# Kernel optimization log

Hardware: AMD Instinct MI355X
Metric: run time of the kernel (lower is better)

Reference implementation:

```python
import jax, jax.numpy as jnp
import numpy as np
from jax import lax

NT, NGRID, NX, H, NY = 365, 2000, 16, 256, 1


def setup_inputs() -> dict:
    key = jax.random.key(0)
    ks = jax.random.split(key, 7)
    s_x = 1.0 / np.sqrt(NX)
    s_h = 1.0 / np.sqrt(H)
    return {
        "x": jax.random.normal(ks[0], (NT, NGRID, NX), dtype=jnp.float32),
        # untied per-gate weights, gate order: [input, forget, cell, output]
        "wx": jax.random.uniform(ks[1], (4, NX, H), jnp.float32, -s_x, s_x),
        "wh": jax.random.uniform(ks[2], (4, H, H), jnp.float32, -s_h, s_h),
        "b": jax.random.uniform(ks[3], (4, H), jnp.float32, -s_h, s_h),
        "w_lin": jax.random.uniform(ks[4], (H, NY), jnp.float32, -s_h, s_h),
        "b_lin": jax.random.uniform(ks[5], (NY,), jnp.float32, -s_h, s_h),
    }


def reference(x, wx, wh, b, w_lin, b_lin):
    # x: [T, N, nx]. Precompute all input-to-gate projections in one big GEMM
    # (the time loop only needs the recurrent h @ wh part).
    ngrid = x.shape[1]
    hid = wh.shape[-1]
    xg = jnp.einsum('tni,gih->tngh', x, wx) + b  # [T, N, 4, H]

    def step(carry, xg_t):
        h, c = carry
        g = xg_t + jnp.einsum('nh,gho->ngo', h, wh)  # [N, 4, H]
        i = jax.nn.sigmoid(g[:, 0])
        f = jax.nn.sigmoid(g[:, 1])
        gt = jnp.tanh(g[:, 2])
        o = jax.nn.sigmoid(g[:, 3])
        c = f * c + i * gt
        h = o * jnp.tanh(c)
        return (h, c), h

    h0 = jnp.zeros((ngrid, hid), dtype=x.dtype)
    c0 = jnp.zeros((ngrid, hid), dtype=x.dtype)
    _, hs = lax.scan(step, (h0, c0), xg)  # hs: [T, N, H]
    out = hs @ w_lin + b_lin  # [T, N, ny]
    return out
```

## Files before the change

### kernel.cpp

```cpp
#include <hip/hip_runtime.h>
#include <cstddef>

#define TSTEPS 365
#define NGRID_ 2000
#define NX_ 16
#define H_ 256
#define CPB 16
#define NBLK (NGRID_ / CPB)

typedef __attribute__((ext_vector_type(8))) short short8v;
typedef __attribute__((ext_vector_type(4))) float f32x4;

__device__ __forceinline__ unsigned short f2bf(float f) {
    unsigned int u = __float_as_uint(f);
    u += 0x7fffu + ((u >> 16) & 1u);
    return (unsigned short)(u >> 16);
}
__device__ __forceinline__ float bf2f(unsigned short s) {
    return __uint_as_float(((unsigned int)s) << 16);
}
__device__ __forceinline__ float sigmoid_f(float v) {
    return 1.0f / (1.0f + __expf(-v));
}
__device__ __forceinline__ float tanh_f(float v) {
    return 1.0f - 2.0f / (__expf(2.0f * v) + 1.0f);
}

#define WH_WORDS (64 * 8 * 64)
#define WX_WORDS (64 * 64)

__global__ __launch_bounds__(256) void pack_weights(
    const float* __restrict__ wh, const float* __restrict__ wx,
    unsigned short* __restrict__ pb)
{
    int tid = blockIdx.x * 256 + threadIdx.x;
    short8v sv;
    if (tid < WH_WORDS) {
        int lane = tid & 63;
        int kt   = (tid >> 6) & 7;
        int gu   = tid >> 9;
        int g    = gu >> 4;
        int ncol = ((gu & 15) << 4) | (lane & 15);
        int kb   = kt * 32 + ((lane >> 4) << 3);
#pragma unroll
        for (int j = 0; j < 8; ++j)
            sv[j] = (short)f2bf(wh[((size_t)(g * H_ + kb + j)) * H_ + ncol]);
        *(short8v*)(pb + (size_t)tid * 8) = sv;
    } else if (tid < WH_WORDS + WX_WORDS) {
        int t2   = tid - WH_WORDS;
        int lane = t2 & 63;
        int gu   = t2 >> 6;
        int g    = gu >> 4;
        int ncol = ((gu & 15) << 4) | (lane & 15);
        int kkb  = (lane >> 4) << 3;
#pragma unroll
        for (int j = 0; j < 8; ++j) {
            int k = (kkb + j) & 15;
            sv[j] = (short)f2bf(wx[((size_t)(g * NX_ + k)) * H_ + ncol]);
        }
        *(short8v*)(pb + (size_t)tid * 8) = sv;
    }
}

__global__ __launch_bounds__(512) void lstm_mfma(
    const float* __restrict__ x,
    const float* __restrict__ b,
    const float* __restrict__ wlin,
    const float* __restrict__ blin,
    const unsigned short* __restrict__ pb,
    float* __restrict__ out)
{
    __shared__ __align__(16) unsigned short Ah[2][32][16][8];
    __shared__ __align__(16) unsigned short Al[2][32][16][8];
    __shared__ __align__(16) unsigned short Ax[2][4][16][8];
    __shared__ float red[2][8][16];

    const int tid = threadIdx.x;
    const int w   = tid >> 6;
    const int l   = tid & 63;
    const int lg  = l >> 4;
    const int ln  = l & 15;
    const int c0  = blockIdx.x * CPB;

    float bias[4][2], wl[2];
#pragma unroll
    for (int g = 0; g < 4; ++g)
#pragma unroll
        for (int ut = 0; ut < 2; ++ut)
            bias[g][ut] = b[g * H_ + w * 32 + ut * 16 + ln];
    wl[0] = wlin[w * 32 + ln];
    wl[1] = wlin[w * 32 + 16 + ln];
    const float bl = blin[0];

    const unsigned short* BX = pb + (size_t)WH_WORDS * 8;

    {
        uint4 z = make_uint4(0, 0, 0, 0);
        ((uint4*)&Ah[0][0][0][0])[tid] = z;
        ((uint4*)&Al[0][0][0][0])[tid] = z;
    }
    if (tid < 256) {
        int cell = tid >> 4, nx = tid & 15;
        float v = x[((size_t)(c0 + cell)) * NX_ + nx];
        unsigned short hi = f2bf(v);
        unsigned short lo = f2bf(v - bf2f(hi));
        Ax[0][nx >> 3][cell][nx & 7] = hi;
        Ax[0][2 + (nx >> 3)][cell][nx & 7] = lo;
    }
    __syncthreads();

    f32x4 acc[4][2];
    float c_st[2][4];
#pragma unroll
    for (int ut = 0; ut < 2; ++ut)
#pragma unroll
        for (int r = 0; r < 4; ++r) c_st[ut][r] = 0.0f;

#pragma unroll 1
    for (int t = 0; t < TSTEPS; ++t) {
        const int rb = t & 1, wb = rb ^ 1;

#pragma unroll
        for (int g = 0; g < 4; ++g)
#pragma unroll
            for (int ut = 0; ut < 2; ++ut) {
                f32x4 a0 = {bias[g][ut], bias[g][ut], bias[g][ut], bias[g][ut]};
                acc[g][ut] = a0;
            }

#pragma unroll
        for (int kt = 0; kt < 8; ++kt) {
            short8v ah = *(const short8v*)&Ah[rb][kt * 4 + lg][ln][0];
            short8v al = *(const short8v*)&Al[rb][kt * 4 + lg][ln][0];
#pragma unroll
            for (int g = 0; g < 4; ++g)
#pragma unroll
                for (int ut = 0; ut < 2; ++ut) {
                    int gu = (g << 4) | (w * 2 + ut);
                    short8v bb = *(const short8v*)(pb + ((size_t)(gu * 8 + kt) * 64 + l) * 8);
                    acc[g][ut] = __builtin_amdgcn_mfma_f32_16x16x32_bf16(ah, bb, acc[g][ut], 0, 0, 0);
                    acc[g][ut] = __builtin_amdgcn_mfma_f32_16x16x32_bf16(al, bb, acc[g][ut], 0, 0, 0);
                }
        }
        {
            short8v axv = *(const short8v*)&Ax[rb][lg][ln][0];
#pragma unroll
            for (int g = 0; g < 4; ++g)
#pragma unroll
                for (int ut = 0; ut < 2; ++ut) {
                    int gu = (g << 4) | (w * 2 + ut);
                    short8v bb = *(const short8v*)(BX + ((size_t)gu * 64 + l) * 8);
                    acc[g][ut] = __builtin_amdgcn_mfma_f32_16x16x32_bf16(axv, bb, acc[g][ut], 0, 0, 0);
                }
        }

        float hN[2][4];
#pragma unroll
        for (int ut = 0; ut < 2; ++ut)
#pragma unroll
            for (int r = 0; r < 4; ++r) {
                float ig = sigmoid_f(acc[0][ut][r]);
                float fg = sigmoid_f(acc[1][ut][r]);
                float gt = tanh_f(acc[2][ut][r]);
                float og = sigmoid_f(acc[3][ut][r]);
                float c  = fmaf(fg, c_st[ut][r], ig * gt);
                c_st[ut][r] = c;
                hN[ut][r]   = og * tanh_f(c);
            }

#pragma unroll
        for (int ut = 0; ut < 2; ++ut) {
            int u = w * 32 + ut * 16 + ln;
            int row = u >> 3, q = u & 7;
#pragma unroll
            for (int r = 0; r < 4; ++r) {
                int cell = lg * 4 + r;
                unsigned short hi = f2bf(hN[ut][r]);
                Ah[wb][row][cell][q] = hi;
                Al[wb][row][cell][q] = f2bf(hN[ut][r] - bf2f(hi));
            }
        }
        if (t + 1 < TSTEPS && tid < 256) {
            int cell = tid >> 4, nx = tid & 15;
            float v = x[(((size_t)(t + 1)) * NGRID_ + c0 + cell) * NX_ + nx];
            unsigned short hi = f2bf(v);
            unsigned short lo = f2bf(v - bf2f(hi));
            Ax[wb][nx >> 3][cell][nx & 7] = hi;
            Ax[wb][2 + (nx >> 3)][cell][nx & 7] = lo;
        }

        {
            float p[4];
#pragma unroll
            for (int r = 0; r < 4; ++r) {
                p[r] = fmaf(hN[0][r], wl[0], hN[1][r] * wl[1]);
#pragma unroll
                for (int off = 1; off < 16; off <<= 1)
                    p[r] += __shfl_xor(p[r], off);
            }
            if (ln == 0) {
#pragma unroll
                for (int r = 0; r < 4; ++r)
                    red[rb][w][lg * 4 + r] = p[r];
            }
        }

        __syncthreads();

        if (tid < CPB) {
            float s = bl;
#pragma unroll
            for (int w2 = 0; w2 < 8; ++w2) s += red[rb][w2][tid];
            out[(size_t)t * NGRID_ + c0 + tid] = s;
        }
    }
}

extern "C" void kernel_launch(void* const* d_in, const int* in_sizes, int n_in,
                              void* d_out, int out_size, void* d_ws, size_t ws_size,
                              hipStream_t stream) {
    const float* x    = (const float*)d_in[0];
    const float* wx   = (const float*)d_in[1];
    const float* wh   = (const float*)d_in[2];
    const float* b    = (const float*)d_in[3];
    const float* wlin = (const float*)d_in[4];
    const float* blin = (const float*)d_in[5];
    float* out = (float*)d_out;
    unsigned short* pb = (unsigned short*)d_ws;

    hipLaunchKernelGGL(pack_weights, dim3((WH_WORDS + WX_WORDS) / 256), dim3(256),
                       0, stream, wh, wx, pb);
    hipLaunchKernelGGL(lstm_mfma, dim3(NBLK), dim3(512), 0, stream,
                       x, b, wlin, blin, pb, out);
}
```

Measured before the change: 4.877 ms.

## Process two 16-cell tiles per block and software-pipeline weight fragment loads

```diff
diff --git a/kernel.cpp b/kernel.cpp
--- a/kernel.cpp
+++ b/kernel.cpp
@@ -5,8 +5,8 @@
 #define NGRID_ 2000
 #define NX_ 16
 #define H_ 256
-#define CPB 16
-#define NBLK (NGRID_ / CPB)
+#define CPB 32
+#define NBLK ((NGRID_ + CPB - 1) / CPB)
 
 typedef __attribute__((ext_vector_type(8))) short short8v;
 typedef __attribute__((ext_vector_type(4))) float f32x4;
@@ -62,7 +62,7 @@
     }
 }
 
-__global__ __launch_bounds__(512) void lstm_mfma(
+__global__ __launch_bounds__(512, 2) void lstm_mfma(
     const float* __restrict__ x,
     const float* __restrict__ b,
     const float* __restrict__ wlin,
@@ -70,10 +70,10 @@
     const unsigned short* __restrict__ pb,
     float* __restrict__ out)
 {
-    __shared__ __align__(16) unsigned short Ah[2][32][16][8];
-    __shared__ __align__(16) unsigned short Al[2][32][16][8];
-    __shared__ __align__(16) unsigned short Ax[2][4][16][8];
-    __shared__ float red[2][8][16];
+    __shared__ __align__(16) unsigned short Ah[2][2][32][16][8];
+    __shared__ __align__(16) unsigned short Al[2][2][32][16][8];
+    __shared__ __align__(16) unsigned short Ax[2][2][4][16][8];
+    __shared__ float red[2][8][2][16];
 
     const int tid = threadIdx.x;
     const int w   = tid >> 6;
@@ -96,124 +96,162 @@
 
     {
         uint4 z = make_uint4(0, 0, 0, 0);
-        ((uint4*)&Ah[0][0][0][0])[tid] = z;
-        ((uint4*)&Al[0][0][0][0])[tid] = z;
-    }
-    if (tid < 256) {
-        int cell = tid >> 4, nx = tid & 15;
-        float v = x[((size_t)(c0 + cell)) * NX_ + nx];
+#pragma unroll
+        for (int i = 0; i < 2; ++i) {
+            ((uint4*)Ah)[tid + i * 512] = z;
+            ((uint4*)Al)[tid + i * 512] = z;
+        }
+    }
+    {
+        const int cell = tid >> 4, nx = tid & 15;
+        const int gc = c0 + cell;
+        float v = (gc < NGRID_) ? x[(size_t)gc * NX_ + nx] : 0.0f;
         unsigned short hi = f2bf(v);
         unsigned short lo = f2bf(v - bf2f(hi));
-        Ax[0][nx >> 3][cell][nx & 7] = hi;
-        Ax[0][2 + (nx >> 3)][cell][nx & 7] = lo;
-    }
+        Ax[0][cell >> 4][nx >> 3][cell & 15][nx & 7] = hi;
+        Ax[0][cell >> 4][2 + (nx >> 3)][cell & 15][nx & 7] = lo;
+    }
+
+    short8v bbA[8], bbB[8], bx[8];
+#pragma unroll
+    for (int i = 0; i < 8; ++i) {
+        int gu = ((i >> 1) << 4) | (w * 2 + (i & 1));
+        bbA[i] = *(const short8v*)(pb + (((size_t)gu * 8 + 0) * 64 + l) * 8);
+        bx[i]  = *(const short8v*)(BX + ((size_t)gu * 64 + l) * 8);
+    }
+
     __syncthreads();
 
-    f32x4 acc[4][2];
-    float c_st[2][4];
-#pragma unroll
-    for (int ut = 0; ut < 2; ++ut)
-#pragma unroll
-        for (int r = 0; r < 4; ++r) c_st[ut][r] = 0.0f;
+    f32x4 acc0[8], acc1[8];
+    float cst[2][2][4];
+#pragma unroll
+    for (int ct = 0; ct < 2; ++ct)
+#pragma unroll
+        for (int ut = 0; ut < 2; ++ut)
+#pragma unroll
+            for (int r = 0; r < 4; ++r) cst[ct][ut][r] = 0.0f;
+
+#define KT_ROUND(KT, CUR, NXT, LOADKT)                                         \
+    {                                                                          \
+        _Pragma("unroll")                                                      \
+        for (int i = 0; i < 8; ++i) {                                          \
+            int gu = ((i >> 1) << 4) | (w * 2 + (i & 1));                      \
+            NXT[i] = *(const short8v*)(pb + (((size_t)gu * 8 + (LOADKT)) * 64 + l) * 8); \
+        }                                                                      \
+        short8v ah0 = *(const short8v*)&Ah[rb][0][(KT) * 4 + lg][ln][0];       \
+        short8v al0 = *(const short8v*)&Al[rb][0][(KT) * 4 + lg][ln][0];       \
+        short8v ah1 = *(const short8v*)&Ah[rb][1][(KT) * 4 + lg][ln][0];       \
+        short8v al1 = *(const short8v*)&Al[rb][1][(KT) * 4 + lg][ln][0];       \
+        _Pragma("unroll")                                                      \
+        for (int i = 0; i < 8; ++i) {                                          \
+            acc0[i] = __builtin_amdgcn_mfma_f32_16x16x32_bf16(ah0, CUR[i], acc0[i], 0, 0, 0); \
+            acc0[i] = __builtin_amdgcn_mfma_f32_16x16x32_bf16(al0, CUR[i], acc0[i], 0, 0, 0); \
+            acc1[i] = __builtin_amdgcn_mfma_f32_16x16x32_bf16(ah1, CUR[i], acc1[i], 0, 0, 0); \
+            acc1[i] = __builtin_amdgcn_mfma_f32_16x16x32_bf16(al1, CUR[i], acc1[i], 0, 0, 0); \
+        }                                                                      \
+    }
 
 #pragma unroll 1
     for (int t = 0; t < TSTEPS; ++t) {
         const int rb = t & 1, wb = rb ^ 1;
 
 #pragma unroll
-        for (int g = 0; g < 4; ++g)
-#pragma unroll
-            for (int ut = 0; ut < 2; ++ut) {
-                f32x4 a0 = {bias[g][ut], bias[g][ut], bias[g][ut], bias[g][ut]};
-                acc[g][ut] = a0;
+        for (int i = 0; i < 8; ++i) {
+            float bv = bias[i >> 1][i & 1];
+            f32x4 a0 = {bv, bv, bv, bv};
+            acc0[i] = a0;
+            acc1[i] = a0;
+        }
+
+        KT_ROUND(0, bbA, bbB, 1)
+        KT_ROUND(1, bbB, bbA, 2)
+        KT_ROUND(2, bbA, bbB, 3)
+        KT_ROUND(3, bbB, bbA, 4)
+        KT_ROUND(4, bbA, bbB, 5)
+        KT_ROUND(5, bbB, bbA, 6)
+        KT_ROUND(6, bbA, bbB, 7)
+        KT_ROUND(7, bbB, bbA, 0)
+
+        {
+            short8v ax0 = *(const short8v*)&Ax[rb][0][lg][ln][0];
+            short8v ax1 = *(const short8v*)&Ax[rb][1][lg][ln][0];
+#pragma unroll
+            for (int i = 0; i < 8; ++i) {
+                acc0[i] = __builtin_amdgcn_mfma_f32_16x16x32_bf16(ax0, bx[i], acc0[i], 0, 0, 0);
+                acc1[i] = __builtin_amdgcn_mfma_f32_16x16x32_bf16(ax1, bx[i], acc1[i], 0, 0, 0);
             }
-
-#pragma unroll
-        for (int kt = 0; kt < 8; ++kt) {
-            short8v ah = *(const short8v*)&Ah[rb][kt * 4 + lg][ln][0];
-            short8v al = *(const short8v*)&Al[rb][kt * 4 + lg][ln][0];
-#pragma unroll
-            for (int g = 0; g < 4; ++g)
-#pragma unroll
-                for (int ut = 0; ut < 2; ++ut) {
-                    int gu = (g << 4) | (w * 2 + ut);
-                    short8v bb = *(const short8v*)(pb + ((size_t)(gu * 8 + kt) * 64 + l) * 8);
-                    acc[g][ut] = __builtin_amdgcn_mfma_f32_16x16x32_bf16(ah, bb, acc[g][ut], 0, 0, 0);
-                    acc[g][ut] = __builtin_amdgcn_mfma_f32_16x16x32_bf16(al, bb, acc[g][ut], 0, 0, 0);
-                }
-        }
-        {
-            short8v axv = *(const short8v*)&Ax[rb][lg][ln][0];
-#pragma unroll
-            for (int g = 0; g < 4; ++g)
-#pragma unroll
-                for (int ut = 0; ut < 2; ++ut) {
-                    int gu = (g << 4) | (w * 2 + ut);
-                    short8v bb = *(const short8v*)(BX + ((size_t)gu * 64 + l) * 8);
-                    acc[g][ut] = __builtin_amdgcn_mfma_f32_16x16x32_bf16(axv, bb, acc[g][ut], 0, 0, 0);
-                }
-        }
-
-        float hN[2][4];
-#pragma unroll
-        for (int ut = 0; ut < 2; ++ut)
-#pragma unroll
-            for (int r = 0; r < 4; ++r) {
-                float ig = sigmoid_f(acc[0][ut][r]);
-                float fg = sigmoid_f(acc[1][ut][r]);
-                float gt = tanh_f(acc[2][ut][r]);
-                float og = sigmoid_f(acc[3][ut][r]);
-                float c  = fmaf(fg, c_st[ut][r], ig * gt);
-                c_st[ut][r] = c;
-                hN[ut][r]   = og * tanh_f(c);
-            }
-
-#pragma unroll
-        for (int ut = 0; ut < 2; ++ut) {
-            int u = w * 32 + ut * 16 + ln;
-            int row = u >> 3, q = u & 7;
-#pragma unroll
-            for (int r = 0; r < 4; ++r) {
-                int cell = lg * 4 + r;
-                unsigned short hi = f2bf(hN[ut][r]);
-                Ah[wb][row][cell][q] = hi;
-                Al[wb][row][cell][q] = f2bf(hN[ut][r] - bf2f(hi));
-            }
-        }
-        if (t + 1 < TSTEPS && tid < 256) {
-            int cell = tid >> 4, nx = tid & 15;
-            float v = x[(((size_t)(t + 1)) * NGRID_ + c0 + cell) * NX_ + nx];
+        }
+
+#define GATES(ACC, CT)                                                         \
+        {                                                                      \
+            float hN[2][4];                                                    \
+            _Pragma("unroll")                                                  \
+            for (int ut = 0; ut < 2; ++ut)                                     \
+                _Pragma("unroll")                                              \
+                for (int r = 0; r < 4; ++r) {                                  \
+                    float ig = sigmoid_f(ACC[0 * 2 + ut][r]);                  \
+                    float fg = sigmoid_f(ACC[1 * 2 + ut][r]);                  \
+                    float gt = tanh_f(ACC[2 * 2 + ut][r]);                     \
+                    float og = sigmoid_f(ACC[3 * 2 + ut][r]);                  \
+                    float c  = fmaf(fg, cst[CT][ut][r], ig * gt);              \
+                    cst[CT][ut][r] = c;                                        \
+                    hN[ut][r] = og * tanh_f(c);                                \
+                }                                                              \
+            _Pragma("unroll")                                                  \
+            for (int ut = 0; ut < 2; ++ut) {                                   \
+                int u = w * 32 + ut * 16 + ln;                                 \
+                _Pragma("unroll")                                              \
+                for (int r = 0; r < 4; ++r) {                                  \
+                    int cell = lg * 4 + r;                                     \
+                    unsigned short hi = f2bf(hN[ut][r]);                       \
+                    Ah[wb][CT][u >> 3][cell][u & 7] = hi;                      \
+                    Al[wb][CT][u >> 3][cell][u & 7] = f2bf(hN[ut][r] - bf2f(hi)); \
+                }                                                              \
+            }                                                                  \
+            float p[4];                                                        \
+            _Pragma("unroll")                                                  \
+            for (int r = 0; r < 4; ++r) {                                      \
+                p[r] = fmaf(hN[0][r], wl[0], hN[1][r] * wl[1]);                \
+                _Pragma("unroll")                                              \
+                for (int off = 1; off < 16; off <<= 1)                         \
+                    p[r] += __shfl_xor(p[r], off);                             \
+            }                                                                  \
+            if (ln == 0) {                                                     \
+                _Pragma("unroll")                                              \
+                for (int r = 0; r < 4; ++r) red[rb][w][CT][lg * 4 + r] = p[r]; \
+            }                                                                  \
+        }
+
+        GATES(acc0, 0)
+        GATES(acc1, 1)
+
+        if (t + 1 < TSTEPS) {
+            const int cell = tid >> 4, nx = tid & 15;
+            const int gc = c0 + cell;
+            float v = (gc < NGRID_)
+                          ? x[(((size_t)(t + 1)) * NGRID_ + gc) * NX_ + nx]
+                          : 0.0f;
             unsigned short hi = f2bf(v);
             unsigned short lo = f2bf(v - bf2f(hi));
-            Ax[wb][nx >> 3][cell][nx & 7] = hi;
-            Ax[wb][2 + (nx >> 3)][cell][nx & 7] = lo;
-        }
-
-        {
-            float p[4];
-#pragma unroll
-            for (int r = 0; r < 4; ++r) {
-                p[r] = fmaf(hN[0][r], wl[0], hN[1][r] * wl[1]);
-#pragma unroll
-                for (int off = 1; off < 16; off <<= 1)
-                    p[r] += __shfl_xor(p[r], off);
+            Ax[wb][cell >> 4][nx >> 3][cell & 15][nx & 7] = hi;
+            Ax[wb][cell >> 4][2 + (nx >> 3)][cell & 15][nx & 7] = lo;
+        }
+
+        __syncthreads();
+
+        if (tid < CPB) {
+            const int gc = c0 + tid;
+            if (gc < NGRID_) {
+                float s = bl;
+#pragma unroll
+                for (int w2 = 0; w2 < 8; ++w2)
+                    s += red[rb][w2][tid >> 4][tid & 15];
+                out[(size_t)t * NGRID_ + gc] = s;
             }
-            if (ln == 0) {
-#pragma unroll
-                for (int r = 0; r < 4; ++r)
-                    red[rb][w][lg * 4 + r] = p[r];
-            }
-        }
-
-        __syncthreads();
-
-        if (tid < CPB) {
-            float s = bl;
-#pragma unroll
-            for (int w2 = 0; w2 < 8; ++w2) s += red[rb][w2][tid];
-            out[(size_t)t * NGRID_ + c0 + tid] = s;
-        }
-    }
+        }
+    }
+#undef KT_ROUND
+#undef GATES
 }
 
 extern "C" void kernel_launch(void* const* d_in, const int* in_sizes, int n_in,
```

Measured after the change: 6.388 ms. 31.0% more time.

## Process 32 cells per block and reuse each weight fragment across two cell tiles

Applied to the files above, without the earlier changes.

```diff
diff --git a/kernel.cpp b/kernel.cpp
--- a/kernel.cpp
+++ b/kernel.cpp
@@ -5,8 +5,8 @@
 #define NGRID_ 2000
 #define NX_ 16
 #define H_ 256
-#define CPB 16
-#define NBLK (NGRID_ / CPB)
+#define CPB 32
+#define NBLK ((NGRID_ + CPB - 1) / CPB)
 
 typedef __attribute__((ext_vector_type(8))) short short8v;
 typedef __attribute__((ext_vector_type(4))) float f32x4;
@@ -70,10 +70,10 @@
     const unsigned short* __restrict__ pb,
     float* __restrict__ out)
 {
-    __shared__ __align__(16) unsigned short Ah[2][32][16][8];
-    __shared__ __align__(16) unsigned short Al[2][32][16][8];
-    __shared__ __align__(16) unsigned short Ax[2][4][16][8];
-    __shared__ float red[2][8][16];
+    __shared__ __align__(16) unsigned short Ah[2][32][32][8];
+    __shared__ __align__(16) unsigned short Al[2][32][32][8];
+    __shared__ __align__(16) unsigned short Ax[2][4][32][8];
+    __shared__ float red[2][8][32];
 
     const int tid = threadIdx.x;
     const int w   = tid >> 6;
@@ -82,12 +82,13 @@
     const int ln  = l & 15;
     const int c0  = blockIdx.x * CPB;
 
-    float bias[4][2], wl[2];
+    float bias[4][2];
 #pragma unroll
     for (int g = 0; g < 4; ++g)
 #pragma unroll
-        for (int ut = 0; ut < 2; ++ut)
-            bias[g][ut] = b[g * H_ + w * 32 + ut * 16 + ln];
+        for (int j = 0; j < 2; ++j)
+            bias[g][j] = b[g * H_ + w * 32 + j * 16 + ln];
+    float wl[2];
     wl[0] = wlin[w * 32 + ln];
     wl[1] = wlin[w * 32 + 16 + ln];
     const float bl = blin[0];
@@ -96,25 +97,53 @@
 
     {
         uint4 z = make_uint4(0, 0, 0, 0);
-        ((uint4*)&Ah[0][0][0][0])[tid] = z;
-        ((uint4*)&Al[0][0][0][0])[tid] = z;
-    }
-    if (tid < 256) {
-        int cell = tid >> 4, nx = tid & 15;
-        float v = x[((size_t)(c0 + cell)) * NX_ + nx];
+        ((uint4*)&Ah[0][0][0][0])[tid]       = z;
+        ((uint4*)&Ah[0][0][0][0])[tid + 512] = z;
+        ((uint4*)&Al[0][0][0][0])[tid]       = z;
+        ((uint4*)&Al[0][0][0][0])[tid + 512] = z;
+    }
+    {
+        const int cell = tid >> 4, nx = tid & 15;
+        const int gc = c0 + cell;
+        float v = (gc < NGRID_) ? x[(size_t)gc * NX_ + nx] : 0.0f;
         unsigned short hi = f2bf(v);
         unsigned short lo = f2bf(v - bf2f(hi));
-        Ax[0][nx >> 3][cell][nx & 7] = hi;
+        Ax[0][nx >> 3][cell][nx & 7]     = hi;
         Ax[0][2 + (nx >> 3)][cell][nx & 7] = lo;
     }
     __syncthreads();
 
-    f32x4 acc[4][2];
-    float c_st[2][4];
-#pragma unroll
-    for (int ut = 0; ut < 2; ++ut)
-#pragma unroll
-        for (int r = 0; r < 4; ++r) c_st[ut][r] = 0.0f;
+    f32x4 acc[4][2][2];
+    float cst[2][2][4];
+#pragma unroll
+    for (int j = 0; j < 2; ++j)
+#pragma unroll
+        for (int ct = 0; ct < 2; ++ct)
+#pragma unroll
+            for (int r = 0; r < 4; ++r) cst[j][ct][r] = 0.0f;
+
+#define KT_ROUND(KT)                                                           \
+    {                                                                          \
+        short8v ah0 = *(const short8v*)&Ah[rb][(KT) * 4 + lg][ln][0];          \
+        short8v al0 = *(const short8v*)&Al[rb][(KT) * 4 + lg][ln][0];          \
+        short8v ah1 = *(const short8v*)&Ah[rb][(KT) * 4 + lg][16 + ln][0];     \
+        short8v al1 = *(const short8v*)&Al[rb][(KT) * 4 + lg][16 + ln][0];     \
+        _Pragma("unroll")                                                      \
+        for (int g = 0; g < 4; ++g) {                                          \
+            short8v b0 = *(const short8v*)(pb +                                \
+                (((size_t)((g << 4) | (w * 2 + 0)) * 8 + (KT)) * 64 + l) * 8); \
+            short8v b1 = *(const short8v*)(pb +                                \
+                (((size_t)((g << 4) | (w * 2 + 1)) * 8 + (KT)) * 64 + l) * 8); \
+            acc[g][0][0] = __builtin_amdgcn_mfma_f32_16x16x32_bf16(ah0, b0, acc[g][0][0], 0, 0, 0); \
+            acc[g][0][0] = __builtin_amdgcn_mfma_f32_16x16x32_bf16(al0, b0, acc[g][0][0], 0, 0, 0); \
+            acc[g][0][1] = __builtin_amdgcn_mfma_f32_16x16x32_bf16(ah1, b0, acc[g][0][1], 0, 0, 0); \
+            acc[g][0][1] = __builtin_amdgcn_mfma_f32_16x16x32_bf16(al1, b0, acc[g][0][1], 0, 0, 0); \
+            acc[g][1][0] = __builtin_amdgcn_mfma_f32_16x16x32_bf16(ah0, b1, acc[g][1][0], 0, 0, 0); \
+            acc[g][1][0] = __builtin_amdgcn_mfma_f32_16x16x32_bf16(al0, b1, acc[g][1][0], 0, 0, 0); \
+            acc[g][1][1] = __builtin_amdgcn_mfma_f32_16x16x32_bf16(ah1, b1, acc[g][1][1], 0, 0, 0); \
+            acc[g][1][1] = __builtin_amdgcn_mfma_f32_16x16x32_bf16(al1, b1, acc[g][1][1], 0, 0, 0); \
+        }                                                                      \
+    }
 
 #pragma unroll 1
     for (int t = 0; t < TSTEPS; ++t) {
@@ -123,97 +152,93 @@
 #pragma unroll
         for (int g = 0; g < 4; ++g)
 #pragma unroll
-            for (int ut = 0; ut < 2; ++ut) {
-                f32x4 a0 = {bias[g][ut], bias[g][ut], bias[g][ut], bias[g][ut]};
-                acc[g][ut] = a0;
-            }
-
-#pragma unroll
-        for (int kt = 0; kt < 8; ++kt) {
-            short8v ah = *(const short8v*)&Ah[rb][kt * 4 + lg][ln][0];
-            short8v al = *(const short8v*)&Al[rb][kt * 4 + lg][ln][0];
-#pragma unroll
-            for (int g = 0; g < 4; ++g)
-#pragma unroll
-                for (int ut = 0; ut < 2; ++ut) {
-                    int gu = (g << 4) | (w * 2 + ut);
-                    short8v bb = *(const short8v*)(pb + ((size_t)(gu * 8 + kt) * 64 + l) * 8);
-                    acc[g][ut] = __builtin_amdgcn_mfma_f32_16x16x32_bf16(ah, bb, acc[g][ut], 0, 0, 0);
-                    acc[g][ut] = __builtin_amdgcn_mfma_f32_16x16x32_bf16(al, bb, acc[g][ut], 0, 0, 0);
+            for (int j = 0; j < 2; ++j) {
+                f32x4 a0 = {bias[g][j], bias[g][j], bias[g][j], bias[g][j]};
+                acc[g][j][0] = a0;
+                acc[g][j][1] = a0;
+            }
+
+        KT_ROUND(0) KT_ROUND(1) KT_ROUND(2) KT_ROUND(3)
+        KT_ROUND(4) KT_ROUND(5) KT_ROUND(6) KT_ROUND(7)
+
+        {
+            short8v ax0 = *(const short8v*)&Ax[rb][lg][ln][0];
+            short8v ax1 = *(const short8v*)&Ax[rb][lg][16 + ln][0];
+#pragma unroll
+            for (int g = 0; g < 4; ++g) {
+                short8v bx0 = *(const short8v*)(BX +
+                    ((size_t)((g << 4) | (w * 2 + 0)) * 64 + l) * 8);
+                short8v bx1 = *(const short8v*)(BX +
+                    ((size_t)((g << 4) | (w * 2 + 1)) * 64 + l) * 8);
+                acc[g][0][0] = __builtin_amdgcn_mfma_f32_16x16x32_bf16(ax0, bx0, acc[g][0][0], 0, 0, 0);
+                acc[g][0][1] = __builtin_amdgcn_mfma_f32_16x16x32_bf16(ax1, bx0, acc[g][0][1], 0, 0, 0);
+                acc[g][1][0] = __builtin_amdgcn_mfma_f32_16x16x32_bf16(ax0, bx1, acc[g][1][0], 0, 0, 0);
+                acc[g][1][1] = __builtin_amdgcn_mfma_f32_16x16x32_bf16(ax1, bx1, acc[g][1][1], 0, 0, 0);
+            }
+        }
+
+        float p[2][4];
+#pragma unroll
+        for (int ct = 0; ct < 2; ++ct)
+#pragma unroll
+            for (int r = 0; r < 4; ++r) p[ct][r] = 0.0f;
+
+#pragma unroll
+        for (int j = 0; j < 2; ++j) {
+            const int u = w * 32 + j * 16 + ln;
+#pragma unroll
+            for (int ct = 0; ct < 2; ++ct)
+#pragma unroll
+                for (int r = 0; r < 4; ++r) {
+                    float ig = sigmoid_f(acc[0][j][ct][r]);
+                    float fg = sigmoid_f(acc[1][j][ct][r]);
+                    float gt = tanh_f(acc[2][j][ct][r]);
+                    float og = sigmoid_f(acc[3][j][ct][r]);
+                    float c  = fmaf(fg, cst[j][ct][r], ig * gt);
+                    cst[j][ct][r] = c;
+                    float h = og * tanh_f(c);
+                    const int cell = ct * 16 + lg * 4 + r;
+                    unsigned short hi = f2bf(h);
+                    Ah[wb][u >> 3][cell][u & 7] = hi;
+                    Al[wb][u >> 3][cell][u & 7] = f2bf(h - bf2f(hi));
+                    p[ct][r] = fmaf(h, wl[j], p[ct][r]);
                 }
         }
-        {
-            short8v axv = *(const short8v*)&Ax[rb][lg][ln][0];
-#pragma unroll
-            for (int g = 0; g < 4; ++g)
-#pragma unroll
-                for (int ut = 0; ut < 2; ++ut) {
-                    int gu = (g << 4) | (w * 2 + ut);
-                    short8v bb = *(const short8v*)(BX + ((size_t)gu * 64 + l) * 8);
-                    acc[g][ut] = __builtin_amdgcn_mfma_f32_16x16x32_bf16(axv, bb, acc[g][ut], 0, 0, 0);
-                }
-        }
-
-        float hN[2][4];
-#pragma unroll
-        for (int ut = 0; ut < 2; ++ut)
+#pragma unroll
+        for (int ct = 0; ct < 2; ++ct)
 #pragma unroll
             for (int r = 0; r < 4; ++r) {
-                float ig = sigmoid_f(acc[0][ut][r]);
-                float fg = sigmoid_f(acc[1][ut][r]);
-                float gt = tanh_f(acc[2][ut][r]);
-                float og = sigmoid_f(acc[3][ut][r]);
-                float c  = fmaf(fg, c_st[ut][r], ig * gt);
-                c_st[ut][r] = c;
-                hN[ut][r]   = og * tanh_f(c);
-            }
-
-#pragma unroll
-        for (int ut = 0; ut < 2; ++ut) {
-            int u = w * 32 + ut * 16 + ln;
-            int row = u >> 3, q = u & 7;
-#pragma unroll
-            for (int r = 0; r < 4; ++r) {
-                int cell = lg * 4 + r;
-                unsigned short hi = f2bf(hN[ut][r]);
-                Ah[wb][row][cell][q] = hi;
-                Al[wb][row][cell][q] = f2bf(hN[ut][r] - bf2f(hi));
-            }
-        }
-        if (t + 1 < TSTEPS && tid < 256) {
-            int cell = tid >> 4, nx = tid & 15;
-            float v = x[(((size_t)(t + 1)) * NGRID_ + c0 + cell) * NX_ + nx];
+#pragma unroll
+                for (int off = 1; off < 16; off <<= 1)
+                    p[ct][r] += __shfl_xor(p[ct][r], off);
+                if (ln == 0) red[rb][w][ct * 16 + lg * 4 + r] = p[ct][r];
+            }
+
+        if (t + 1 < TSTEPS) {
+            const int cell = tid >> 4, nx = tid & 15;
+            const int gc = c0 + cell;
+            float v = (gc < NGRID_)
+                          ? x[(((size_t)(t + 1)) * NGRID_ + gc) * NX_ + nx]
+                          : 0.0f;
             unsigned short hi = f2bf(v);
             unsigned short lo = f2bf(v - bf2f(hi));
-            Ax[wb][nx >> 3][cell][nx & 7] = hi;
+            Ax[wb][nx >> 3][cell][nx & 7]       = hi;
             Ax[wb][2 + (nx >> 3)][cell][nx & 7] = lo;
         }
 
-        {
-            float p[4];
-#pragma unroll
-            for (int r = 0; r < 4; ++r) {
-                p[r] = fmaf(hN[0][r], wl[0], hN[1][r] * wl[1]);
-#pragma unroll
-                for (int off = 1; off < 16; off <<= 1)
-                    p[r] += __shfl_xor(p[r], off);
-            }
-            if (ln == 0) {
-#pragma unroll
-                for (int r = 0; r < 4; ++r)
-                    red[rb][w][lg * 4 + r] = p[r];
-            }
-        }
-
         __syncthreads();
 
         if (tid < CPB) {
-            float s = bl;
-#pragma unroll
-            for (int w2 = 0; w2 < 8; ++w2) s += red[rb][w2][tid];
-            out[(size_t)t * NGRID_ + c0 + tid] = s;
-        }
-    }
+            const int gc = c0 + tid;
+            if (gc < NGRID_) {
+                float s = bl;
+#pragma unroll
+                for (int w2 = 0; w2 < 8; ++w2) s += red[rb][w2][tid];
+                out[(size_t)t * NGRID_ + gc] = s;
+            }
+        }
+    }
+#undef KT_ROUND
 }
 
 extern "C" void kernel_launch(void* const* d_in, const int* in_sizes, int n_in,
```

Measured after the change: 6.335 ms. +29.9%, slower.
